# Performance work log

Hardware: AMD Instinct MI355X
Metric: run time of the kernel (lower is better)

The kernel has to match this reference:

```python
import jax, jax.numpy as jnp
import numpy as np

NEG_SLOPE = 0.01
EPS = 1e-5


def _p(key, shape, scale=0.05):
    return jax.random.normal(key, shape, dtype=jnp.float32) * scale


def setup_inputs() -> dict:
    key = jax.random.key(0)
    ks = jax.random.split(key, 20)
    B, C0, N = 256, 160, 1024
    trees = jax.random.normal(ks[0], (B, C0, N), dtype=jnp.float32)
    indexes = jax.random.randint(ks[1], (B, 3 * N), 0, N)
    nodes = jax.random.randint(ks[2], (B,), 1, N + 1)
    dims = [(160, 256), (256, 128), (128, 64)]
    inp = {"trees": trees, "indexes": indexes, "nodes": nodes}
    for i, (ci, co) in enumerate(dims, start=1):
        inp[f"Wc{i}"] = _p(ks[2 + 4 * i], (co, ci, 3))   # tree-conv weight
        inp[f"bc{i}"] = jnp.zeros((co,), jnp.float32)
        inp[f"Wm{i}"] = _p(ks[3 + 4 * i], (co, ci))       # channel-mixer (1x1) weight
        inp[f"bm{i}"] = jnp.zeros((co,), jnp.float32)
    inp["W1"] = _p(ks[16], (64, 32))
    inp["b1"] = jnp.zeros((32,), jnp.float32)
    inp["W2"] = _p(ks[17], (32, 1))
    inp["b2"] = jnp.zeros((1,), jnp.float32)
    return inp


def _lero_block(x, idx, Wc, bc, Wm, bm):
    # x: [B, C, N], idx: [B, 3N] gather indices into node axis
    B, C, N = x.shape
    g = jnp.take_along_axis(x, idx[:, None, :], axis=2)          # [B, C, 3N]
    g = g.reshape(B, C, N, 3)                                    # parent/left/right triples
    y = jnp.einsum('bcnk,ock->bon', g, Wc) + bc[None, :, None]   # BinaryTreeConv
    mu = jnp.mean(y, axis=(1, 2), keepdims=True)                 # TreeLayerNorm (per-tree)
    sd = jnp.std(y, axis=(1, 2), keepdims=True, ddof=1)
    y = (y - mu) / (sd + EPS)
    xm = jnp.einsum('bcn,oc->bon', x, Wm) + bm[None, :, None]    # ChannelMixer
    return jax.nn.leaky_relu(xm + y, NEG_SLOPE)


def reference(trees, indexes, nodes,
              Wc1, bc1, Wm1, bm1,
              Wc2, bc2, Wm2, bm2,
              Wc3, bc3, Wm3, bm3,
              W1, b1, W2, b2):
    x = _lero_block(trees, indexes, Wc1, bc1, Wm1, bm1)
    x = _lero_block(x, indexes, Wc2, bc2, Wm2, bm2)
    x = _lero_block(x, indexes, Wc3, bc3, Wm3, bm3)   # [B, 64, N]
    N = x.shape[2]
    mask = jnp.arange(N)[None, :] < nodes[:, None]     # PreciseMaxPooling: mask padding
    pooled = jnp.max(jnp.where(mask[:, None, :], x, -jnp.inf), axis=2)  # [B, 64]
    h = jax.nn.leaky_relu(pooled @ W1 + b1, NEG_SLOPE)
    return h @ W2 + b2                                  # [B, 1]
```

## Files before the change

kernel.cpp:

```cpp
#include <hip/hip_runtime.h>
#include <stdint.h>

using f16 = _Float16;
typedef __attribute__((ext_vector_type(8))) f16 f16x8;
typedef __attribute__((ext_vector_type(4))) f16 f16x4;
typedef __attribute__((ext_vector_type(4))) float f32x4;

constexpr int N = 1024;

__device__ __forceinline__ float leaky(float v) { return v >= 0.f ? v : 0.01f * v; }

__device__ __forceinline__ void dma16(const void* g, void* l) {
    __builtin_amdgcn_global_load_lds(
        (const __attribute__((address_space(1))) uint32_t*)g,
        (__attribute__((address_space(3))) uint32_t*)l, 16, 0, 0);
}

template<int CI, int CO, int SEGS, int NSTG, int UW, bool ISMIX>
__global__ __launch_bounds__(512) void gemm_kernel(
    const f16* __restrict__ X, const int* __restrict__ idx,
    const f16* __restrict__ Wf, const float* __restrict__ bias,
    f16* __restrict__ Y, float2* __restrict__ part,
    const float2* __restrict__ stats)
{
    constexpr int SKT = SEGS * CI / 32;
    constexpr int KS32 = SKT / NSTG;
    constexpr int Ug = CO / 16;
    constexpr int NGRAN = KS32 * UW * 64;
    constexpr int SBYTES = NGRAN * 16;
    constexpr int EBYTES = 8 * 16 * 68 * 4;
    constexpr int LBYTES = SBYTES > EBYTES ? SBYTES : EBYTES;
    static_assert(CI % 32 == 0 && SKT % NSTG == 0 && UW % 4 == 0, "geometry");

    __shared__ alignas(16) char ldsraw[LBYTES];
    __shared__ float redu[16];

    const int tid = threadIdx.x;
    const int w = tid >> 6, l = tid & 63;
    const int n0 = blockIdx.x * 256;
    const int u0 = blockIdx.y * UW;
    const int b  = blockIdx.z;
    const int g  = blockIdx.x + gridDim.x * blockIdx.y;

    int rows[2][SEGS];
    #pragma unroll
    for (int rt = 0; rt < 2; ++rt) {
        int n = n0 + 32 * w + 16 * rt + (l & 15);
        if constexpr (ISMIX) {
            rows[rt][0] = n;
        } else {
            const int* ip = idx + (size_t)b * 3 * N + 3 * n;
            #pragma unroll
            for (int s = 0; s < SEGS; ++s) rows[rt][s] = ip[s];
        }
    }
    const f16* xb = X + (size_t)b * N * CI;
    const int koff = 8 * (l >> 4);

    float2 st = make_float2(0.f, 0.f);
    if constexpr (ISMIX) st = stats[b];

    const f16* lds = (const f16*)ldsraw;

    auto stageW = [&](int pp) {
        for (int gg = tid; gg < NGRAN; gg += 512) {
            int skk = gg / (UW * 64);
            int uu = (gg >> 6) % UW;
            int ll = gg & 63;
            dma16(Wf + (((size_t)(pp * KS32 + skk) * Ug + u0 + uu) * 64 + ll) * 8,
                  ldsraw + (size_t)gg * 16);
        }
    };

    auto loadA = [&](int sk, f16x8& o0, f16x8& o1) {
        const int seg = (sk * 32) / CI;
        const int co = sk * 32 - seg * CI + koff;
        o0 = *(const f16x8*)(xb + (size_t)rows[0][seg] * CI + co);
        o1 = *(const f16x8*)(xb + (size_t)rows[1][seg] * CI + co);
    };

    if constexpr (NSTG == 1) stageW(0);

    constexpr int D = SKT < 3 ? SKT : 3;
    f16x8 pa0[3], pa1[3];
    #pragma unroll
    for (int d = 0; d < D; ++d) loadA(d, pa0[d], pa1[d]);

    if constexpr (NSTG == 1) __syncthreads();

    f32x4 acc[2][UW] = {};

    #pragma unroll
    for (int pp = 0; pp < NSTG; ++pp) {
        if constexpr (NSTG > 1) { stageW(pp); __syncthreads(); }

        #pragma unroll
        for (int skl = 0; skl < KS32; ++skl) {
            const int sk = pp * KS32 + skl;
            f16x8 av0 = pa0[sk % 3], av1 = pa1[sk % 3];
            if (sk + 3 < SKT) loadA(sk + 3, pa0[sk % 3], pa1[sk % 3]);
            #pragma unroll
            for (int uu = 0; uu < UW; ++uu) {
                f16x8 wv = *(const f16x8*)(lds + ((size_t)(skl * UW + uu) * 64 + l) * 8);
                acc[0][uu] = __builtin_amdgcn_mfma_f32_16x16x32_f16(av0, wv, acc[0][uu], 0, 0, 0);
                acc[1][uu] = __builtin_amdgcn_mfma_f32_16x16x32_f16(av1, wv, acc[1][uu], 0, 0, 0);
            }
        }
        if (pp + 1 < NSTG) __syncthreads();
    }

    __syncthreads();

    float (*ep)[68] = (float(*)[68])(ldsraw + w * 4352);
    float ps1 = 0.f, ps2 = 0.f;

    #pragma unroll
    for (int rt = 0; rt < 2; ++rt) {
        #pragma unroll
        for (int E = 0; E < UW / 4; ++E) {
            asm volatile("s_waitcnt lgkmcnt(0)" ::: "memory");
            #pragma unroll
            for (int u4 = 0; u4 < 4; ++u4)
                #pragma unroll
                for (int j = 0; j < 4; ++j)
                    ep[4 * (l >> 4) + j][u4 * 16 + (l & 15)] = acc[rt][E * 4 + u4][j];
            asm volatile("s_waitcnt lgkmcnt(0)" ::: "memory");
            __builtin_amdgcn_sched_barrier(0);
            #pragma unroll
            for (int ci = 0; ci < 2; ++ci) {
                int c = l + 64 * ci;
                int r = c >> 3, oc = (c & 7) * 8;
                int ob = u0 * 16 + E * 64 + oc;
                int n = n0 + 32 * w + 16 * rt + r;
                size_t yoff = ((size_t)b * N + n) * CO + ob;
                float v[8];
                #pragma unroll
                for (int k = 0; k < 8; ++k) v[k] = ep[r][oc + k] + bias[ob + k];
                f16x8 rv;
                if constexpr (!ISMIX) {
                    #pragma unroll
                    for (int k = 0; k < 8; ++k) {
                        ps1 += v[k]; ps2 += v[k] * v[k];
                        rv[k] = (f16)v[k];
                    }
                } else {
                    f16x8 yc = *(const f16x8*)(Y + yoff);
                    #pragma unroll
                    for (int k = 0; k < 8; ++k)
                        rv[k] = (f16)leaky(v[k] + ((float)yc[k] - st.x) * st.y);
                }
                *(f16x8*)(Y + yoff) = rv;
            }
        }
    }

    if constexpr (!ISMIX) {
        #pragma unroll
        for (int m = 32; m; m >>= 1) { ps1 += __shfl_xor(ps1, m); ps2 += __shfl_xor(ps2, m); }
        if (l == 0) { redu[w * 2] = ps1; redu[w * 2 + 1] = ps2; }
        __syncthreads();
        if (tid == 0) {
            float t1 = 0.f, t2 = 0.f;
            #pragma unroll
            for (int k = 0; k < 8; ++k) { t1 += redu[2 * k]; t2 += redu[2 * k + 1]; }
            part[(size_t)b * 16 + g] = make_float2(t1, t2);
        }
    }
}

__global__ __launch_bounds__(64) void reduce_stats_kernel(
    const float2* __restrict__ part, float2* __restrict__ stats, int nparts, float Mf)
{
    int b = blockIdx.x;
    float s1 = 0.f, s2 = 0.f;
    for (int i = threadIdx.x; i < nparts; i += 64) {
        float2 p = part[(size_t)b * 16 + i];
        s1 += p.x; s2 += p.y;
    }
    #pragma unroll
    for (int m = 32; m; m >>= 1) { s1 += __shfl_xor(s1, m); s2 += __shfl_xor(s2, m); }
    if (threadIdx.x == 0) {
        float mu = s1 / Mf;
        float var = (s2 - s1 * s1 / Mf) / (Mf - 1.f);
        var = fmaxf(var, 0.f);
        stats[b] = make_float2(mu, 1.f / (sqrtf(var) + 1e-5f));
    }
}

__global__ __launch_bounds__(256) void transpose_kernel(
    const float* __restrict__ trees, f16* __restrict__ X0)
{
    __shared__ f16 tile[32][68];
    int b = blockIdx.z, c0 = blockIdx.y * 32, n0 = blockIdx.x * 64;
    int tid = threadIdx.x;
    #pragma unroll
    for (int r = 0; r < 2; ++r) {
        int s = tid + 256 * r;
        int c = s >> 4, nq = (s & 15) * 4;
        float4 v = *(const float4*)&trees[((size_t)b * 160 + c0 + c) * N + n0 + nq];
        f16x4 h; h[0] = (f16)v.x; h[1] = (f16)v.y; h[2] = (f16)v.z; h[3] = (f16)v.w;
        *(f16x4*)&tile[c][nq] = h;
    }
    __syncthreads();
    int nn = tid >> 2, gc = tid & 3;
    f16x8 pack;
    #pragma unroll
    for (int e = 0; e < 8; ++e) pack[e] = tile[gc * 8 + e][nn];
    *(f16x8*)(X0 + ((size_t)b * N + n0 + nn) * 160 + c0 + gc * 8) = pack;
}

__device__ __forceinline__ void prepW_one(
    const float* __restrict__ Wsrc, f16* __restrict__ out,
    int e, int CO, int CI, int isconv)
{
    int j = e & 7, l = (e >> 3) & 63, r = e >> 9;
    int U = CO / 16;
    int u = r % U, t = r / U;
    int kap = 32 * t + 8 * (l >> 4) + j;
    int o = 16 * u + (l & 15);
    float v = isconv ? Wsrc[((size_t)o * CI + (kap % CI)) * 3 + kap / CI]
                     : Wsrc[(size_t)o * CI + kap];
    out[e] = (f16)v;
}

__global__ __launch_bounds__(256) void prepW6_kernel(
    const float* Wc1, const float* Wm1, const float* Wc2, const float* Wm2,
    const float* Wc3, const float* Wm3,
    f16* o1, f16* m1, f16* o2, f16* m2, f16* o3, f16* m3)
{
    int bx = blockIdx.x;
    if (bx < 480)       prepW_one(Wc1, o1, (bx -    0) * 256 + threadIdx.x, 256, 160, 1);
    else if (bx < 640)  prepW_one(Wm1, m1, (bx -  480) * 256 + threadIdx.x, 256, 160, 0);
    else if (bx < 1024) prepW_one(Wc2, o2, (bx -  640) * 256 + threadIdx.x, 128, 256, 1);
    else if (bx < 1152) prepW_one(Wm2, m2, (bx - 1024) * 256 + threadIdx.x, 128, 256, 0);
    else if (bx < 1248) prepW_one(Wc3, o3, (bx - 1152) * 256 + threadIdx.x,  64, 128, 1);
    else                prepW_one(Wm3, m3, (bx - 1248) * 256 + threadIdx.x,  64, 128, 0);
}

__global__ __launch_bounds__(256) void final_kernel(
    const f16* __restrict__ x3, const int* __restrict__ nodes,
    const float* __restrict__ W1, const float* __restrict__ b1,
    const float* __restrict__ W2, const float* __restrict__ b2,
    float* __restrict__ out)
{
    int b = blockIdx.x, tid = threadIdx.x;
    int oq = (tid & 7) * 8, rr = tid >> 3;
    int nv = nodes[b];
    const f16* p = x3 + (size_t)b * N * 64 + oq;
    float mx[8];
    #pragma unroll
    for (int k = 0; k < 8; ++k) mx[k] = -3.4e38f;
    for (int n = rr; n < nv; n += 32) {
        f16x8 v = *(const f16x8*)(p + (size_t)n * 64);
        #pragma unroll
        for (int k = 0; k < 8; ++k) mx[k] = fmaxf(mx[k], (float)v[k]);
    }
    __shared__ float pool[32][64];
    __shared__ float pooled[64], hbuf[32];
    #pragma unroll
    for (int k = 0; k < 8; ++k) pool[rr][oq + k] = mx[k];
    __syncthreads();
    if (tid < 64) {
        float m = pool[0][tid];
        #pragma unroll 8
        for (int r = 1; r < 32; ++r) m = fmaxf(m, pool[r][tid]);
        pooled[tid] = m;
    }
    __syncthreads();
    if (tid < 32) {
        float h = b1[tid];
        #pragma unroll 8
        for (int oo = 0; oo < 64; ++oo) h += pooled[oo] * W1[oo * 32 + tid];
        hbuf[tid] = leaky(h);
    }
    __syncthreads();
    if (tid == 0) {
        float rr2 = b2[0];
        for (int jj = 0; jj < 32; ++jj) rr2 += hbuf[jj] * W2[jj];
        out[b] = rr2;
    }
}

extern "C" void kernel_launch(void* const* d_in, const int* in_sizes, int n_in,
                              void* d_out, int out_size, void* d_ws, size_t ws_size,
                              hipStream_t stream)
{
    (void)in_sizes; (void)n_in; (void)out_size; (void)ws_size;
    const float* trees = (const float*)d_in[0];
    const int* indexes = (const int*)d_in[1];
    const int* nodes   = (const int*)d_in[2];
    const float* Wc1 = (const float*)d_in[3];
    const float* bc1 = (const float*)d_in[4];
    const float* Wm1 = (const float*)d_in[5];
    const float* bm1 = (const float*)d_in[6];
    const float* Wc2 = (const float*)d_in[7];
    const float* bc2 = (const float*)d_in[8];
    const float* Wm2 = (const float*)d_in[9];
    const float* bm2 = (const float*)d_in[10];
    const float* Wc3 = (const float*)d_in[11];
    const float* bc3 = (const float*)d_in[12];
    const float* Wm3 = (const float*)d_in[13];
    const float* bm3 = (const float*)d_in[14];
    const float* W1 = (const float*)d_in[15];
    const float* b1 = (const float*)d_in[16];
    const float* W2 = (const float*)d_in[17];
    const float* b2 = (const float*)d_in[18];
    float* out = (float*)d_out;

    char* ws = (char*)d_ws;
    f16* X0 = (f16*)ws;
    f16* A1 = (f16*)(ws + 83886080);
    f16* A2 = (f16*)ws;
    f16* A3 = A1;
    size_t toff = 218103808;
    f16* Wfc1 = (f16*)(ws + toff); toff += (size_t)480 * 256 * 2;
    f16* Wfm1 = (f16*)(ws + toff); toff += (size_t)160 * 256 * 2;
    f16* Wfc2 = (f16*)(ws + toff); toff += (size_t)768 * 128 * 2;
    f16* Wfm2 = (f16*)(ws + toff); toff += (size_t)256 * 128 * 2;
    f16* Wfc3 = (f16*)(ws + toff); toff += (size_t)384 * 64 * 2;
    f16* Wfm3 = (f16*)(ws + toff); toff += (size_t)128 * 64 * 2;
    float2* part  = (float2*)(ws + toff); toff += (size_t)256 * 16 * 8;
    float2* stats = (float2*)(ws + toff);

    transpose_kernel<<<dim3(16, 5, 256), 256, 0, stream>>>(trees, X0);
    prepW6_kernel<<<1280, 256, 0, stream>>>(Wc1, Wm1, Wc2, Wm2, Wc3, Wm3,
                                            Wfc1, Wfm1, Wfc2, Wfm2, Wfc3, Wfm3);

    gemm_kernel<160, 256, 3, 3, 8, false><<<dim3(4, 2, 256), 512, 0, stream>>>(
        X0, indexes, Wfc1, bc1, A1, part, nullptr);
    reduce_stats_kernel<<<256, 64, 0, stream>>>(part, stats, 8, 262144.f);
    gemm_kernel<160, 256, 1, 1, 8, true><<<dim3(4, 2, 256), 512, 0, stream>>>(
        X0, nullptr, Wfm1, bm1, A1, nullptr, stats);

    gemm_kernel<256, 128, 3, 4, 8, false><<<dim3(4, 1, 256), 512, 0, stream>>>(
        A1, indexes, Wfc2, bc2, A2, part, nullptr);
    reduce_stats_kernel<<<256, 64, 0, stream>>>(part, stats, 4, 131072.f);
    gemm_kernel<256, 128, 1, 1, 4, true><<<dim3(4, 2, 256), 512, 0, stream>>>(
        A1, nullptr, Wfm2, bm2, A2, nullptr, stats);

    gemm_kernel<128, 64, 3, 1, 4, false><<<dim3(4, 1, 256), 512, 0, stream>>>(
        A2, indexes, Wfc3, bc3, A3, part, nullptr);
    reduce_stats_kernel<<<256, 64, 0, stream>>>(part, stats, 4, 65536.f);
    gemm_kernel<128, 64, 1, 1, 4, true><<<dim3(4, 1, 256), 512, 0, stream>>>(
        A2, nullptr, Wfm3, bm3, A3, nullptr, stats);

    final_kernel<<<256, 256, 0, stream>>>(A3, nodes, W1, b1, W2, b2, out);
}
```

Measured before the change: 470.6 us.

## Fuse stats reduction into mixer GEMM and widen layer-1 conv tile

Removes the separate reduce_stats kernel launches by having each mixer GEMM thread reduce the per-tree partial sums and compute mean and inverse std directly. Adds an RT template parameter so the layer-1 tree-conv can cover all 256 output channels per block with one row tile, avoiding a duplicate gather of the input across two channel blocks. This trades larger per-block LDS weight staging and lower occupancy for fewer launches and less redundant gathered-load traffic.

After: 462.6 us. About the same (-1.7%).

```diff
diff --git a/kernel.cpp b/kernel.cpp
--- a/kernel.cpp
+++ b/kernel.cpp
@@ -16,12 +16,12 @@
         (__attribute__((address_space(3))) uint32_t*)l, 16, 0, 0);
 }
 
-template<int CI, int CO, int SEGS, int NSTG, int UW, bool ISMIX>
+template<int CI, int CO, int SEGS, int NSTG, int UW, int RT, bool ISMIX>
 __global__ __launch_bounds__(512) void gemm_kernel(
     const f16* __restrict__ X, const int* __restrict__ idx,
     const f16* __restrict__ Wf, const float* __restrict__ bias,
     f16* __restrict__ Y, float2* __restrict__ part,
-    const float2* __restrict__ stats)
+    const float2* __restrict__ pin, int nparts, float Mf)
 {
     constexpr int SKT = SEGS * CI / 32;
     constexpr int KS32 = SKT / NSTG;
@@ -31,21 +31,22 @@
     constexpr int EBYTES = 8 * 16 * 68 * 4;
     constexpr int LBYTES = SBYTES > EBYTES ? SBYTES : EBYTES;
     static_assert(CI % 32 == 0 && SKT % NSTG == 0 && UW % 4 == 0, "geometry");
+    static_assert(RT == 1 || RT == 2, "rt");
 
     __shared__ alignas(16) char ldsraw[LBYTES];
     __shared__ float redu[16];
 
     const int tid = threadIdx.x;
     const int w = tid >> 6, l = tid & 63;
-    const int n0 = blockIdx.x * 256;
+    const int n0 = blockIdx.x * (128 * RT);
     const int u0 = blockIdx.y * UW;
     const int b  = blockIdx.z;
     const int g  = blockIdx.x + gridDim.x * blockIdx.y;
 
-    int rows[2][SEGS];
-    #pragma unroll
-    for (int rt = 0; rt < 2; ++rt) {
-        int n = n0 + 32 * w + 16 * rt + (l & 15);
+    int rows[RT][SEGS];
+    #pragma unroll
+    for (int rt = 0; rt < RT; ++rt) {
+        int n = n0 + 16 * (RT * w + rt) + (l & 15);
         if constexpr (ISMIX) {
             rows[rt][0] = n;
         } else {
@@ -58,7 +59,16 @@
     const int koff = 8 * (l >> 4);
 
     float2 st = make_float2(0.f, 0.f);
-    if constexpr (ISMIX) st = stats[b];
+    if constexpr (ISMIX) {
+        float s1 = 0.f, s2 = 0.f;
+        for (int i = 0; i < nparts; ++i) {
+            float2 p = pin[(size_t)b * 16 + i];
+            s1 += p.x; s2 += p.y;
+        }
+        float mu = s1 / Mf;
+        float var = fmaxf((s2 - s1 * s1 / Mf) / (Mf - 1.f), 0.f);
+        st = make_float2(mu, 1.f / (sqrtf(var) + 1e-5f));
+    }
 
     const f16* lds = (const f16*)ldsraw;
 
@@ -72,23 +82,24 @@
         }
     };
 
-    auto loadA = [&](int sk, f16x8& o0, f16x8& o1) {
+    f16x8 pa[RT][3];
+    auto loadA = [&](int sk, int d) {
         const int seg = (sk * 32) / CI;
         const int co = sk * 32 - seg * CI + koff;
-        o0 = *(const f16x8*)(xb + (size_t)rows[0][seg] * CI + co);
-        o1 = *(const f16x8*)(xb + (size_t)rows[1][seg] * CI + co);
+        #pragma unroll
+        for (int rt = 0; rt < RT; ++rt)
+            pa[rt][d] = *(const f16x8*)(xb + (size_t)rows[rt][seg] * CI + co);
     };
 
     if constexpr (NSTG == 1) stageW(0);
 
     constexpr int D = SKT < 3 ? SKT : 3;
-    f16x8 pa0[3], pa1[3];
-    #pragma unroll
-    for (int d = 0; d < D; ++d) loadA(d, pa0[d], pa1[d]);
+    #pragma unroll
+    for (int d = 0; d < D; ++d) loadA(d, d);
 
     if constexpr (NSTG == 1) __syncthreads();
 
-    f32x4 acc[2][UW] = {};
+    f32x4 acc[RT][UW] = {};
 
     #pragma unroll
     for (int pp = 0; pp < NSTG; ++pp) {
@@ -97,13 +108,16 @@
         #pragma unroll
         for (int skl = 0; skl < KS32; ++skl) {
             const int sk = pp * KS32 + skl;
-            f16x8 av0 = pa0[sk % 3], av1 = pa1[sk % 3];
-            if (sk + 3 < SKT) loadA(sk + 3, pa0[sk % 3], pa1[sk % 3]);
+            f16x8 av[RT];
+            #pragma unroll
+            for (int rt = 0; rt < RT; ++rt) av[rt] = pa[rt][sk % 3];
+            if (sk + 3 < SKT) loadA(sk + 3, sk % 3);
             #pragma unroll
             for (int uu = 0; uu < UW; ++uu) {
                 f16x8 wv = *(const f16x8*)(lds + ((size_t)(skl * UW + uu) * 64 + l) * 8);
-                acc[0][uu] = __builtin_amdgcn_mfma_f32_16x16x32_f16(av0, wv, acc[0][uu], 0, 0, 0);
-                acc[1][uu] = __builtin_amdgcn_mfma_f32_16x16x32_f16(av1, wv, acc[1][uu], 0, 0, 0);
+                #pragma unroll
+                for (int rt = 0; rt < RT; ++rt)
+                    acc[rt][uu] = __builtin_amdgcn_mfma_f32_16x16x32_f16(av[rt], wv, acc[rt][uu], 0, 0, 0);
             }
         }
         if (pp + 1 < NSTG) __syncthreads();
@@ -115,7 +129,7 @@
     float ps1 = 0.f, ps2 = 0.f;
 
     #pragma unroll
-    for (int rt = 0; rt < 2; ++rt) {
+    for (int rt = 0; rt < RT; ++rt) {
         #pragma unroll
         for (int E = 0; E < UW / 4; ++E) {
             asm volatile("s_waitcnt lgkmcnt(0)" ::: "memory");
@@ -131,7 +145,7 @@
                 int c = l + 64 * ci;
                 int r = c >> 3, oc = (c & 7) * 8;
                 int ob = u0 * 16 + E * 64 + oc;
-                int n = n0 + 32 * w + 16 * rt + r;
+                int n = n0 + 16 * (RT * w + rt) + r;
                 size_t yoff = ((size_t)b * N + n) * CO + ob;
                 float v[8];
                 #pragma unroll
@@ -165,25 +179,6 @@
             for (int k = 0; k < 8; ++k) { t1 += redu[2 * k]; t2 += redu[2 * k + 1]; }
             part[(size_t)b * 16 + g] = make_float2(t1, t2);
         }
-    }
-}
-
-__global__ __launch_bounds__(64) void reduce_stats_kernel(
-    const float2* __restrict__ part, float2* __restrict__ stats, int nparts, float Mf)
-{
-    int b = blockIdx.x;
-    float s1 = 0.f, s2 = 0.f;
-    for (int i = threadIdx.x; i < nparts; i += 64) {
-        float2 p = part[(size_t)b * 16 + i];
-        s1 += p.x; s2 += p.y;
-    }
-    #pragma unroll
-    for (int m = 32; m; m >>= 1) { s1 += __shfl_xor(s1, m); s2 += __shfl_xor(s2, m); }
-    if (threadIdx.x == 0) {
-        float mu = s1 / Mf;
-        float var = (s2 - s1 * s1 / Mf) / (Mf - 1.f);
-        var = fmaxf(var, 0.f);
-        stats[b] = make_float2(mu, 1.f / (sqrtf(var) + 1e-5f));
     }
 }
 
@@ -319,30 +314,26 @@
     f16* Wfm2 = (f16*)(ws + toff); toff += (size_t)256 * 128 * 2;
     f16* Wfc3 = (f16*)(ws + toff); toff += (size_t)384 * 64 * 2;
     f16* Wfm3 = (f16*)(ws + toff); toff += (size_t)128 * 64 * 2;
-    float2* part  = (float2*)(ws + toff); toff += (size_t)256 * 16 * 8;
-    float2* stats = (float2*)(ws + toff);
+    float2* part  = (float2*)(ws + toff);
 
     transpose_kernel<<<dim3(16, 5, 256), 256, 0, stream>>>(trees, X0);
     prepW6_kernel<<<1280, 256, 0, stream>>>(Wc1, Wm1, Wc2, Wm2, Wc3, Wm3,
                                             Wfc1, Wfm1, Wfc2, Wfm2, Wfc3, Wfm3);
 
-    gemm_kernel<160, 256, 3, 3, 8, false><<<dim3(4, 2, 256), 512, 0, stream>>>(
-        X0, indexes, Wfc1, bc1, A1, part, nullptr);
-    reduce_stats_kernel<<<256, 64, 0, stream>>>(part, stats, 8, 262144.f);
-    gemm_kernel<160, 256, 1, 1, 8, true><<<dim3(4, 2, 256), 512, 0, stream>>>(
-        X0, nullptr, Wfm1, bm1, A1, nullptr, stats);
-
-    gemm_kernel<256, 128, 3, 4, 8, false><<<dim3(4, 1, 256), 512, 0, stream>>>(
-        A1, indexes, Wfc2, bc2, A2, part, nullptr);
-    reduce_stats_kernel<<<256, 64, 0, stream>>>(part, stats, 4, 131072.f);
-    gemm_kernel<256, 128, 1, 1, 4, true><<<dim3(4, 2, 256), 512, 0, stream>>>(
-        A1, nullptr, Wfm2, bm2, A2, nullptr, stats);
-
-    gemm_kernel<128, 64, 3, 1, 4, false><<<dim3(4, 1, 256), 512, 0, stream>>>(
-        A2, indexes, Wfc3, bc3, A3, part, nullptr);
-    reduce_stats_kernel<<<256, 64, 0, stream>>>(part, stats, 4, 65536.f);
-    gemm_kernel<128, 64, 1, 1, 4, true><<<dim3(4, 1, 256), 512, 0, stream>>>(
-        A2, nullptr, Wfm3, bm3, A3, nullptr, stats);
+    gemm_kernel<160, 256, 3, 3, 16, 1, false><<<dim3(8, 1, 256), 512, 0, stream>>>(
+        X0, indexes, Wfc1, bc1, A1, part, nullptr, 0, 0.f);
+    gemm_kernel<160, 256, 1, 1, 8, 2, true><<<dim3(4, 2, 256), 512, 0, stream>>>(
+        X0, nullptr, Wfm1, bm1, A1, nullptr, part, 8, 262144.f);
+
+    gemm_kernel<256, 128, 3, 4, 8, 2, false><<<dim3(4, 1, 256), 512, 0, stream>>>(
+        A1, indexes, Wfc2, bc2, A2, part, nullptr, 0, 0.f);
+    gemm_kernel<256, 128, 1, 1, 4, 2, true><<<dim3(4, 2, 256), 512, 0, stream>>>(
+        A1, nullptr, Wfm2, bm2, A2, nullptr, part, 4, 131072.f);
+
+    gemm_kernel<128, 64, 3, 1, 4, 2, false><<<dim3(4, 1, 256), 512, 0, stream>>>(
+        A2, indexes, Wfc3, bc3, A3, part, nullptr, 0, 0.f);
+    gemm_kernel<128, 64, 1, 1, 4, 2, true><<<dim3(4, 1, 256), 512, 0, stream>>>(
+        A2, nullptr, Wfm3, bm3, A3, nullptr, part, 4, 65536.f);
 
     final_kernel<<<256, 256, 0, stream>>>(A3, nodes, W1, b1, W2, b2, out);
 }
```
